# Performance work log

Measured on AMD Instinct MI355X. Metric: run time of the kernel, lower is better.

The kernel has to match this reference:

```python
import jax, jax.numpy as jnp
import numpy as np

S, DIM, E, K = 16384, 4096, 64, 2

def setup_inputs() -> dict:
    key = jax.random.key(0)
    kx, kw = jax.random.split(key)
    x = jax.random.normal(kx, (S, DIM), dtype=jnp.float32)
    W = jax.random.normal(kw, (E, DIM), dtype=jnp.float32) * (1.0 / np.sqrt(DIM))
    b = jnp.zeros((E,), dtype=jnp.float32)
    return {"x": x, "W": W, "b": b}

def reference(x, W, b):
    # Router linear: [S, dim] @ [dim, E] + [E] -> [S, E]
    logits = jnp.einsum('sd,ed->se', x, W) + b
    probs = jax.nn.softmax(logits, axis=-1)              # [S, E]
    topk_vals, topk_idx = jax.lax.top_k(probs, K)        # [S, K], [S, K]
    # Load-balance aux loss (Switch Transformer style)
    importance = probs.mean(axis=0)                      # [E]
    hard1 = topk_idx[:, 0]                               # [S]
    load = jax.ops.segment_sum(jnp.ones((S,), dtype=probs.dtype), hard1,
                               num_segments=E) / max(S, 1)
    aux_loss = E * jnp.sum(importance * load)
    return (topk_idx, topk_vals, aux_loss)
```

## Files before the change

kernel.cpp:

```cpp
#include <hip/hip_runtime.h>
#include <hip/hip_bf16.h>

#define SROWS 16384
#define DIMK  4096
#define NE    64
#define BM    16
#define NBLK  (SROWS/BM)
#define KSEG  1024
#define NSTEP 16
#define SBK   64
#define WSPLIT_SHORTS 262144
#define WSOFF_F 262144
#define WSOFF2  (WSOFF_F + NBLK*64)

typedef __attribute__((ext_vector_type(8))) short short8;
typedef __attribute__((ext_vector_type(4))) float f32x4;

__device__ __forceinline__ void split8(const float4 a, const float4 c, short8& hi, short8& lo) {
    float f[8] = {a.x, a.y, a.z, a.w, c.x, c.y, c.z, c.w};
    #pragma unroll
    for (int i = 0; i < 8; ++i) {
        unsigned short h = __bfloat16_as_ushort(__float2bfloat16(f[i]));
        float hf = __uint_as_float((unsigned)h << 16);
        unsigned short l = __bfloat16_as_ushort(__float2bfloat16(f[i] - hf));
        hi[i] = (short)h;
        lo[i] = (short)l;
    }
}

__global__ void w_split(const float* __restrict__ W, unsigned short* __restrict__ wsp)
{
    const int idx   = blockIdx.x * 256 + threadIdx.x;
    const int kslot = idx & 511;
    const int e     = idx >> 9;
    const float* p = W + (size_t)e * DIMK + kslot * 8;
    float4 va = *reinterpret_cast<const float4*>(p);
    float4 vb = *reinterpret_cast<const float4*>(p + 4);
    short8 hi, lo;
    split8(va, vb, hi, lo);
    *reinterpret_cast<short8*>(wsp + (size_t)(kslot * 64 + e) * 8)                 = hi;
    *reinterpret_cast<short8*>(wsp + WSPLIT_SHORTS + (size_t)(kslot * 64 + e) * 8) = lo;
}

__device__ __forceinline__ void gl_lds16(const void* g, void* l) {
    __builtin_amdgcn_global_load_lds(
        (const __attribute__((address_space(1))) void*)g,
        (__attribute__((address_space(3))) void*)l, 16, 0, 0);
}

__global__ __launch_bounds__(256, 4) void gate_main(
    const float* __restrict__ x, const unsigned short* __restrict__ wsp,
    const float* __restrict__ b, float* __restrict__ out, float* __restrict__ ws)
{
    __shared__ __align__(16) char smem[32768];

    const int tid  = threadIdx.x;
    const int lane = tid & 63;
    const int ksw  = __builtin_amdgcn_readfirstlane(tid >> 6);
    const int row0 = blockIdx.x * BM;

    const float* xsq[4];
    #pragma unroll
    for (int q = 0; q < 4; ++q) {
        const int rowq = q * 4 + (lane >> 4);
        const int gs   = (lane & 15) ^ (rowq & 7);
        xsq[q] = x + (size_t)(row0 + rowq) * DIMK + ksw * KSEG + gs * 4;
    }
    char* const slab = smem + ksw * 8192;

    auto STAGE = [&](int st, int bsel) {
        char* xb = slab + bsel * 4096;
        #pragma unroll
        for (int q = 0; q < 4; ++q)
            gl_lds16(xsq[q] + (size_t)st * SBK, xb + q * 1024 + lane * 16);
    };

    f32x4 acc[4];
    #pragma unroll
    for (int n = 0; n < 4; ++n) acc[n] = (f32x4){0.f, 0.f, 0.f, 0.f};

    const int rm = lane & 7;
    const char* xrow = slab + (lane & 15) * 256;
    const unsigned short* wBbase = wsp + ((size_t)(ksw * 128) * 64) * 8;

    STAGE(0, 0);

    #pragma unroll 1
    for (int st = 0; st < NSTEP; ++st) {
        asm volatile("s_waitcnt vmcnt(0)" ::: "memory");
        __builtin_amdgcn_sched_barrier(0);
        if (st + 1 < NSTEP) STAGE(st + 1, (st + 1) & 1);

        const char* xb = xrow + (st & 1) * 4096;

        #pragma unroll
        for (int c2 = 0; c2 < 2; ++c2) {
            const int ga = c2 * 8 + 2 * (lane >> 4);
            float4 xa = *reinterpret_cast<const float4*>(xb + ((ga    ) ^ rm) * 16);
            float4 xc = *reinterpret_cast<const float4*>(xb + ((ga + 1) ^ rm) * 16);
            short8 ah, al;
            split8(xa, xc, ah, al);

            const int ksl = st * 8 + c2 * 4 + (lane >> 4);
            const unsigned short* bp = wBbase + ((size_t)ksl * 64 + (lane & 15)) * 8;
            short8 bh[4], bl[4];
            #pragma unroll
            for (int n = 0; n < 4; ++n) {
                bh[n] = *reinterpret_cast<const short8*>(bp + n * 128);
                bl[n] = *reinterpret_cast<const short8*>(bp + WSPLIT_SHORTS + n * 128);
            }

            #pragma unroll
            for (int n = 0; n < 4; ++n)
                acc[n] = __builtin_amdgcn_mfma_f32_16x16x32_bf16(ah, bh[n], acc[n], 0, 0, 0);
            #pragma unroll
            for (int n = 0; n < 4; ++n)
                acc[n] = __builtin_amdgcn_mfma_f32_16x16x32_bf16(ah, bl[n], acc[n], 0, 0, 0);
            #pragma unroll
            for (int n = 0; n < 4; ++n)
                acc[n] = __builtin_amdgcn_mfma_f32_16x16x32_bf16(al, bh[n], acc[n], 0, 0, 0);
        }
    }

    __syncthreads();

    float* const part = reinterpret_cast<float*>(smem);
    float* const Lb   = reinterpret_cast<float*>(smem + 12288);
    float* const red  = reinterpret_cast<float*>(smem + 17792);

    if (ksw > 0) {
        #pragma unroll
        for (int n = 0; n < 4; ++n)
            #pragma unroll
            for (int j = 0; j < 4; ++j)
                part[(ksw - 1) * 1024 + lane * 16 + n * 4 + j] = acc[n][j];
    }
    __syncthreads();
    if (ksw == 0) {
        #pragma unroll
        for (int n = 0; n < 4; ++n) {
            #pragma unroll
            for (int j = 0; j < 4; ++j) {
                float v = acc[n][j]
                        + part[0 * 1024 + lane * 16 + n * 4 + j]
                        + part[1 * 1024 + lane * 16 + n * 4 + j]
                        + part[2 * 1024 + lane * 16 + n * 4 + j];
                const int e  = n * 16 + (lane & 15);
                const int rl = (lane >> 4) * 4 + j;
                Lb[e * 17 + rl] = v;
            }
        }
    }
    __syncthreads();

    float impAcc = 0.f, cntAcc = 0.f;
    const float blane = b[lane];
    float* outIdx = out;
    float* outVal = out + (size_t)SROWS * 2;

    #pragma unroll 1
    for (int rr = 0; rr < 4; ++rr) {
        const int r = ksw * 4 + rr;
        const float logit = Lb[lane * 17 + r] + blane;

        float v1 = logit; int i1 = lane;
        #pragma unroll
        for (int off = 32; off; off >>= 1) {
            float ov = __shfl_xor(v1, off);
            int   oi = __shfl_xor(i1, off);
            if (ov > v1 || (ov == v1 && oi < i1)) { v1 = ov; i1 = oi; }
        }
        float p = expf(logit - v1);
        float ssum = p;
        #pragma unroll
        for (int off = 32; off; off >>= 1) ssum += __shfl_xor(ssum, off);

        float v2 = (lane == i1) ? -3.402823466e38f : logit;
        int i2 = lane;
        #pragma unroll
        for (int off = 32; off; off >>= 1) {
            float ov = __shfl_xor(v2, off);
            int   oi = __shfl_xor(i2, off);
            if (ov > v2 || (ov == v2 && oi < i2)) { v2 = ov; i2 = oi; }
        }

        impAcc += p / ssum;
        cntAcc += (i1 == lane) ? 1.f : 0.f;

        if (lane == 0) {
            const int sr = row0 + r;
            outIdx[sr * 2 + 0] = (float)i1;
            outIdx[sr * 2 + 1] = (float)i2;
            outVal[sr * 2 + 0] = 1.f / ssum;
            outVal[sr * 2 + 1] = expf(v2 - v1) / ssum;
        }
    }

    __syncthreads();
    red[ksw * 64 + lane]       = impAcc;
    red[256 + ksw * 64 + lane] = cntAcc;
    __syncthreads();
    if (tid < 64) {
        float si = 0.f, sc2 = 0.f;
        #pragma unroll
        for (int g = 0; g < 4; ++g) {
            si  += red[g * 64 + tid];
            sc2 += red[256 + g * 64 + tid];
        }
        ws[WSOFF_F + (size_t)blockIdx.x * 64 + tid] = si;
        ws[WSOFF2  + (size_t)blockIdx.x * 64 + tid] = sc2;
    }
}

__global__ void gate_reduce(const float* __restrict__ ws, float* __restrict__ out)
{
    __shared__ float li[64 * 64], lc[64 * 64];
    const int t = threadIdx.x;
    const int g  = t >> 4;
    const int e4 = (t & 15) * 4;
    float4 si = make_float4(0.f, 0.f, 0.f, 0.f);
    float4 sc = make_float4(0.f, 0.f, 0.f, 0.f);
    const int base = g * 16;
    #pragma unroll 4
    for (int bb = base; bb < base + 16; ++bb) {
        float4 a = *reinterpret_cast<const float4*>(&ws[WSOFF_F + (size_t)bb * 64 + e4]);
        float4 c = *reinterpret_cast<const float4*>(&ws[WSOFF2  + (size_t)bb * 64 + e4]);
        si.x += a.x; si.y += a.y; si.z += a.z; si.w += a.w;
        sc.x += c.x; sc.y += c.y; sc.z += c.z; sc.w += c.w;
    }
    *reinterpret_cast<float4*>(&li[g * 64 + e4]) = si;
    *reinterpret_cast<float4*>(&lc[g * 64 + e4]) = sc;
    __syncthreads();
    if (t < 64) {
        float ti = 0.f, tc = 0.f;
        #pragma unroll 8
        for (int gg = 0; gg < 64; ++gg) { ti += li[gg * 64 + t]; tc += lc[gg * 64 + t]; }
        li[t] = ti * tc;
    }
    __syncthreads();
    if (t == 0) {
        float s = 0.f;
        for (int i = 0; i < NE; ++i) s += li[i];
        out[(size_t)SROWS * 4] = s * ((float)NE / ((float)SROWS * (float)SROWS));
    }
}

extern "C" void kernel_launch(void* const* d_in, const int* in_sizes, int n_in,
                              void* d_out, int out_size, void* d_ws, size_t ws_size,
                              hipStream_t stream)
{
    const float* x = (const float*)d_in[0];
    const float* W = (const float*)d_in[1];
    const float* b = (const float*)d_in[2];
    float* out = (float*)d_out;
    unsigned short* wsp = (unsigned short*)d_ws;
    float* wsf = (float*)d_ws;

    w_split<<<128, 256, 0, stream>>>(W, wsp);
    gate_main<<<NBLK, 256, 0, stream>>>(x, wsp, b, out, wsf);
    gate_reduce<<<1, 1024, 0, stream>>>(wsf, out);
}
```

Before: 82.13 us.

## Load x directly into registers with one-step prefetch instead of LDS staging

Removes the global_load_lds double-buffered staging of x through shared memory. Each lane now loads its own 32-float slices straight into registers and prefetches the next step's slices while the current step runs its MFMAs. This drops the LDS round-trip, the swizzled LDS reads and the per-step vmcnt(0) wait, and shrinks shared memory to what the epilogue needs. The cost is more vector registers for the prefetch buffers and a prefetch depth of one step. Coalescing is also weaker, since each row's 256 bytes per step are now fetched by four lanes with two loads each.

```diff
diff --git a/kernel.cpp b/kernel.cpp
--- a/kernel.cpp
+++ b/kernel.cpp
@@ -8,7 +8,6 @@
 #define NBLK  (SROWS/BM)
 #define KSEG  1024
 #define NSTEP 16
-#define SBK   64
 #define WSPLIT_SHORTS 262144
 #define WSOFF_F 262144
 #define WSOFF2  (WSOFF_F + NBLK*64)
@@ -42,64 +41,48 @@
     *reinterpret_cast<short8*>(wsp + WSPLIT_SHORTS + (size_t)(kslot * 64 + e) * 8) = lo;
 }
 
-__device__ __forceinline__ void gl_lds16(const void* g, void* l) {
-    __builtin_amdgcn_global_load_lds(
-        (const __attribute__((address_space(1))) void*)g,
-        (__attribute__((address_space(3))) void*)l, 16, 0, 0);
-}
-
 __global__ __launch_bounds__(256, 4) void gate_main(
     const float* __restrict__ x, const unsigned short* __restrict__ wsp,
     const float* __restrict__ b, float* __restrict__ out, float* __restrict__ ws)
 {
-    __shared__ __align__(16) char smem[32768];
+    __shared__ float smem[4672];
+    float* const part = smem;
+    float* const Lb   = smem + 3072;
+    float* const red  = smem + 4160;
 
     const int tid  = threadIdx.x;
     const int lane = tid & 63;
     const int ksw  = __builtin_amdgcn_readfirstlane(tid >> 6);
     const int row0 = blockIdx.x * BM;
 
-    const float* xsq[4];
-    #pragma unroll
-    for (int q = 0; q < 4; ++q) {
-        const int rowq = q * 4 + (lane >> 4);
-        const int gs   = (lane & 15) ^ (rowq & 7);
-        xsq[q] = x + (size_t)(row0 + rowq) * DIMK + ksw * KSEG + gs * 4;
-    }
-    char* const slab = smem + ksw * 8192;
-
-    auto STAGE = [&](int st, int bsel) {
-        char* xb = slab + bsel * 4096;
-        #pragma unroll
-        for (int q = 0; q < 4; ++q)
-            gl_lds16(xsq[q] + (size_t)st * SBK, xb + q * 1024 + lane * 16);
-    };
+    const float* xA = x + (size_t)(row0 + (lane & 15)) * DIMK
+                        + ksw * KSEG + (lane >> 4) * 8;
+    const unsigned short* wBbase = wsp + ((size_t)(ksw * 128) * 64) * 8;
 
     f32x4 acc[4];
     #pragma unroll
     for (int n = 0; n < 4; ++n) acc[n] = (f32x4){0.f, 0.f, 0.f, 0.f};
 
-    const int rm = lane & 7;
-    const char* xrow = slab + (lane & 15) * 256;
-    const unsigned short* wBbase = wsp + ((size_t)(ksw * 128) * 64) * 8;
-
-    STAGE(0, 0);
+    float4 a00 = *reinterpret_cast<const float4*>(xA);
+    float4 a01 = *reinterpret_cast<const float4*>(xA + 4);
+    float4 a10 = *reinterpret_cast<const float4*>(xA + 32);
+    float4 a11 = *reinterpret_cast<const float4*>(xA + 36);
 
     #pragma unroll 1
     for (int st = 0; st < NSTEP; ++st) {
-        asm volatile("s_waitcnt vmcnt(0)" ::: "memory");
+        const int pst = (st + 1 < NSTEP) ? st + 1 : NSTEP - 1;
+        const float* xp = xA + (size_t)pst * 64;
+        float4 p00 = *reinterpret_cast<const float4*>(xp);
+        float4 p01 = *reinterpret_cast<const float4*>(xp + 4);
+        float4 p10 = *reinterpret_cast<const float4*>(xp + 32);
+        float4 p11 = *reinterpret_cast<const float4*>(xp + 36);
         __builtin_amdgcn_sched_barrier(0);
-        if (st + 1 < NSTEP) STAGE(st + 1, (st + 1) & 1);
-
-        const char* xb = xrow + (st & 1) * 4096;
 
         #pragma unroll
         for (int c2 = 0; c2 < 2; ++c2) {
-            const int ga = c2 * 8 + 2 * (lane >> 4);
-            float4 xa = *reinterpret_cast<const float4*>(xb + ((ga    ) ^ rm) * 16);
-            float4 xc = *reinterpret_cast<const float4*>(xb + ((ga + 1) ^ rm) * 16);
             short8 ah, al;
-            split8(xa, xc, ah, al);
+            if (c2 == 0) split8(a00, a01, ah, al);
+            else         split8(a10, a11, ah, al);
 
             const int ksl = st * 8 + c2 * 4 + (lane >> 4);
             const unsigned short* bp = wBbase + ((size_t)ksl * 64 + (lane & 15)) * 8;
@@ -120,13 +103,12 @@
             for (int n = 0; n < 4; ++n)
                 acc[n] = __builtin_amdgcn_mfma_f32_16x16x32_bf16(al, bh[n], acc[n], 0, 0, 0);
         }
-    }
-
-    __syncthreads();
-
-    float* const part = reinterpret_cast<float*>(smem);
-    float* const Lb   = reinterpret_cast<float*>(smem + 12288);
-    float* const red  = reinterpret_cast<float*>(smem + 17792);
+
+        __builtin_amdgcn_sched_barrier(0);
+        a00 = p00; a01 = p01; a10 = p10; a11 = p11;
+    }
+
+    __syncthreads();
 
     if (ksw > 0) {
         #pragma unroll
```

New measurement: 94.89 us. +15.5%, slower.
